# Performance work log

Hardware: AMD Instinct MI355X
Metric: run time of the kernel (lower is better)

## Reference

```python
import jax, jax.numpy as jnp
import numpy as np

B, N = 2, 2048
D_MODEL, HEADS = 512, 8
D_K = D_MODEL // HEADS
D_HIDDEN = 2048
MIN_SPREAD = 2.0
MIN_RBF = 1e-3
MAX_RBF = 1.0
LN_EPS = 1e-5


def setup_inputs() -> dict:
    key = jax.random.key(0)
    ks = jax.random.split(key, 12)
    xs = (6.0 / (D_K + D_MODEL)) ** 0.5
    q = jax.random.normal(ks[0], (B, N, D_MODEL), dtype=jnp.float32)
    k = jax.random.normal(ks[1], (B, N, D_MODEL), dtype=jnp.float32)
    v = jax.random.normal(ks[2], (B, N, D_MODEL), dtype=jnp.float32)
    coords = jax.random.normal(ks[3], (B, N, 3), dtype=jnp.float32) * 10.0
    mask = jnp.ones((B, N), dtype=bool)
    q_proj = jax.random.uniform(ks[4], (HEADS, D_MODEL, D_K), minval=-xs, maxval=xs)
    k_proj = jax.random.uniform(ks[5], (HEADS, D_MODEL, D_K), minval=-xs, maxval=xs)
    v_proj = jax.random.uniform(ks[6], (HEADS, D_MODEL, D_K), minval=-xs, maxval=xs)
    q_bias = jnp.zeros((HEADS, D_K))
    k_bias = jnp.zeros((HEADS, D_K))
    v_bias = jnp.zeros((HEADS, D_K))
    ow = (1.0 / D_MODEL) ** 0.5
    out_w = jax.random.uniform(ks[7], (D_MODEL, D_MODEL), minval=-ow, maxval=ow)
    spread_w = jnp.zeros((HEADS,))
    beta_w = jnp.zeros((HEADS,))
    ln1_g = jnp.ones((D_MODEL,)); ln1_b = jnp.zeros((D_MODEL,))
    ln2_g = jnp.ones((D_MODEL,)); ln2_b = jnp.zeros((D_MODEL,))
    w1 = jax.random.normal(ks[8], (D_MODEL, D_HIDDEN)) * 0.02
    b1 = jnp.zeros((D_HIDDEN,))
    w2 = jax.random.normal(ks[9], (D_HIDDEN, D_MODEL)) * 0.02
    b2 = jnp.zeros((D_MODEL,))
    return dict(q=q, k=k, v=v, coords=coords, mask=mask,
                q_proj=q_proj, k_proj=k_proj, v_proj=v_proj,
                q_bias=q_bias, k_bias=k_bias, v_bias=v_bias,
                out_w=out_w, spread_w=spread_w, beta_w=beta_w,
                ln1_g=ln1_g, ln1_b=ln1_b, ln2_g=ln2_g, ln2_b=ln2_b,
                w1=w1, b1=b1, w2=w2, b2=b2)


def _layernorm(x, g, b):
    mu = jnp.mean(x, axis=-1, keepdims=True)
    var = jnp.mean((x - mu) ** 2, axis=-1, keepdims=True)
    return (x - mu) * jax.lax.rsqrt(var + LN_EPS) * g + b


def _geo_attention(q, k, v, coords, mask,
                   q_proj, k_proj, v_proj, q_bias, k_bias, v_bias,
                   out_w, spread_w, beta_w):
    # per-head projections: [B,H,N,dk]
    Q = jnp.einsum('bnd,hdk->bhnk', q, q_proj) + q_bias[None, :, None, :]
    K = jnp.einsum('bnd,hdk->bhnk', k, k_proj) + k_bias[None, :, None, :]
    V = jnp.einsum('bnd,hdk->bhnk', v, v_proj) + v_bias[None, :, None, :]

    spreads = MIN_SPREAD + jnp.exp(spread_w)   # [H]
    betas = jnp.exp(beta_w)                    # [H]

    # pairwise squared distances [B,N,N]
    d2 = jnp.sum((coords[:, :, None, :] - coords[:, None, :, :]) ** 2, axis=-1)
    # per-head Gaussian RBF [B,H,N,N]
    rbf = jnp.exp(-d2[:, None, :, :] / (2.0 * spreads[None, :, None, None] ** 2))

    scores = jnp.einsum('bhnk,bhmk->bhnm', Q, K) / jnp.sqrt(jnp.float32(D_K))
    scores = betas[None, :, None, None] * rbf * scores

    # sparsity: keys with rbf outside [min_rbf, max_rbf] or padded are masked out
    valid = (rbf >= MIN_RBF) & (rbf <= MAX_RBF) & mask[:, None, None, :]
    scores = jnp.where(valid, scores, -jnp.inf)
    attn = jax.nn.softmax(scores, axis=-1)     # diagonal always valid (rbf=1)

    out = jnp.einsum('bhnm,bhmk->bhnk', attn, V)         # [B,H,N,dk]
    # torch: out.permute(0,2,3,1).reshape(B,N,d_model) -> (b,n,dk,h) layout
    out = jnp.transpose(out, (0, 2, 3, 1)).reshape(out.shape[0], out.shape[2], D_MODEL)
    return out @ out_w.T


def reference(q, k, v, coords, mask,
              q_proj, k_proj, v_proj, q_bias, k_bias, v_bias,
              out_w, spread_w, beta_w,
              ln1_g, ln1_b, ln2_g, ln2_b, w1, b1, w2, b2):
    attn_out = _geo_attention(q, k, v, coords, mask,
                              q_proj, k_proj, v_proj, q_bias, k_bias, v_bias,
                              out_w, spread_w, beta_w)
    x = _layernorm(q + attn_out, ln1_g, ln1_b)
    ffn = jax.nn.relu(x @ w1 + b1) @ w2 + b2
    x = _layernorm(x + ffn, ln2_g, ln2_b)
    return x
```

## Files before the change

kernel.cpp:

```cpp
#include <hip/hip_runtime.h>
#include <math.h>

typedef __attribute__((ext_vector_type(8))) short bf16x8;
typedef __attribute__((ext_vector_type(4))) float f32x4;

#define MFMA16(a,b,c) __builtin_amdgcn_mfma_f32_16x16x32_bf16((a),(b),(c),0,0,0)

__device__ __forceinline__ unsigned short f2bf(float f) {
    union { float f; unsigned u; } x; x.f = f;
    unsigned r = x.u + 0x7FFFu + ((x.u >> 16) & 1u);
    return (unsigned short)(r >> 16);
}

__device__ __forceinline__ unsigned cvt_pk_bf16(float lo, float hi) {
    unsigned r;
    asm("v_cvt_pk_bf16_f32 %0, %1, %2" : "=v"(r) : "v"(lo), "v"(hi));
    return r;
}

__global__ __launch_bounds__(256) void cvt_qkv(
    const float* __restrict__ q, const float* __restrict__ k,
    const float* __restrict__ v,
    unsigned short* __restrict__ qb, unsigned short* __restrict__ kb,
    unsigned short* __restrict__ vb, int n)
{
    for (int i = blockIdx.x * 256 + threadIdx.x; i < n; i += gridDim.x * 256) {
        qb[i] = f2bf(q[i]); kb[i] = f2bf(k[i]); vb[i] = f2bf(v[i]);
    }
}

__global__ __launch_bounds__(256) void cvt_weights(
    const float* __restrict__ qp, const float* __restrict__ kp,
    const float* __restrict__ vp, const float* __restrict__ ow,
    const float* __restrict__ w1, const float* __restrict__ w2,
    const float* __restrict__ qbias, const float* __restrict__ kbias,
    const float* __restrict__ vbias,
    unsigned short* __restrict__ qpT, unsigned short* __restrict__ kpT,
    unsigned short* __restrict__ vpT, unsigned short* __restrict__ owT,
    unsigned short* __restrict__ w1T, unsigned short* __restrict__ w2T,
    float* __restrict__ biasC)
{
    const int NP = 262144;
    const int total = 4 * NP + 1048576 + 1048576 + 1536;
    for (int i = blockIdx.x * 256 + threadIdx.x; i < total; i += gridDim.x * 256) {
        if (i < 3 * NP) {
            int which = i / NP, r = i - which * NP;
            int n = r >> 9, d = r & 511;
            int h = n >> 6, kk = n & 63;
            const float* src = (which == 0) ? qp : (which == 1) ? kp : vp;
            unsigned short* dst = (which == 0) ? qpT : (which == 1) ? kpT : vpT;
            dst[r] = f2bf(src[(h << 15) + (d << 6) + kk]);
        } else if (i < 4 * NP) {
            int r = i - 3 * NP;
            int oi = r >> 9, f = r & 511;
            int h = f >> 6, kk = f & 63;
            owT[r] = f2bf(ow[(oi << 9) + (kk << 3) + h]);
        } else if (i < 4 * NP + 1048576) {
            int r = i - 4 * NP;
            int n = r >> 9, d = r & 511;
            w1T[r] = f2bf(w1[(d << 11) + n]);
        } else if (i < 4 * NP + 2097152) {
            int r = i - 4 * NP - 1048576;
            int n = r >> 11, d = r & 2047;
            w2T[r] = f2bf(w2[(d << 9) + n]);
        } else {
            int j = i - 4 * NP - 2097152;
            biasC[j] = (j < 512) ? qbias[j] : (j < 1024) ? kbias[j - 512] : vbias[j - 1024];
        }
    }
}

template<int BNT, int RELU, int SF32, int SB16, int SVTR, int SQKV>
__global__ __launch_bounds__(256) void gemm_bt(
    const unsigned short* __restrict__ Aq,
    const unsigned short* __restrict__ Ak,
    const unsigned short* __restrict__ Av,
    const unsigned short* __restrict__ Bt,
    const float* __restrict__ bias,
    float* __restrict__ Cf, unsigned short* __restrict__ Cb,
    unsigned short* __restrict__ Cb2, unsigned short* __restrict__ Cb3,
    int M, int N, int K)
{
    constexpr int BC = BNT / 32;
    __shared__ unsigned short As[128][72];
    __shared__ unsigned short Bs[BNT][72];
    const int tid = threadIdx.x;
    const int m0 = blockIdx.y << 7, n0 = blockIdx.x * BNT;
    const int wv = tid >> 6, lane = tid & 63;
    const int lrow = lane & 15, kg = lane >> 4;
    const int wr = (wv >> 1) << 6, wc = (wv & 1) * (BNT / 2);

    const unsigned short* A = Aq;
    if (SQKV) A = (n0 < 512) ? Aq : (n0 < 1024) ? Ak : Av;

    f32x4 acc[4][BC];
    const f32x4 z4 = {0.f, 0.f, 0.f, 0.f};
#pragma unroll
    for (int i = 0; i < 4; ++i)
#pragma unroll
        for (int j = 0; j < BC; ++j) acc[i][j] = z4;

    const int nkt = K >> 6;
    for (int kt = 0; kt < nkt; ++kt) {
        __syncthreads();
        const int k0 = kt << 6;
#pragma unroll
        for (int i = 0; i < 4; ++i) {
            int slot = tid + (i << 8);
            int r = slot >> 3, c = (slot & 7) << 3;
            *(int4*)(&As[r][c]) = *(const int4*)(&A[(long)(m0 + r) * K + k0 + c]);
        }
#pragma unroll
        for (int i = 0; i < BC; ++i) {
            int slot = tid + (i << 8);
            int r = slot >> 3, c = (slot & 7) << 3;
            *(int4*)(&Bs[r][c]) = *(const int4*)(&Bt[(long)(n0 + r) * K + k0 + c]);
        }
        __syncthreads();
#pragma unroll
        for (int ks = 0; ks < 2; ++ks) {
            const int koff = (ks << 5) + (kg << 3);
            bf16x8 af[4], bfr[BC];
#pragma unroll
            for (int mi = 0; mi < 4; ++mi)
                af[mi] = *(const bf16x8*)(&As[wr + (mi << 4) + lrow][koff]);
#pragma unroll
            for (int ni = 0; ni < BC; ++ni)
                bfr[ni] = *(const bf16x8*)(&Bs[wc + (ni << 4) + lrow][koff]);
#pragma unroll
            for (int mi = 0; mi < 4; ++mi)
#pragma unroll
                for (int ni = 0; ni < BC; ++ni)
                    acc[mi][ni] = MFMA16(af[mi], bfr[ni], acc[mi][ni]);
        }
    }

#pragma unroll
    for (int mi = 0; mi < 4; ++mi) {
#pragma unroll
        for (int ni = 0; ni < BC; ++ni) {
            const int col = n0 + wc + (ni << 4) + lrow;
            const float bv = bias ? bias[col] : 0.0f;
#pragma unroll
            for (int j = 0; j < 4; ++j) {
                const int row = m0 + wr + (mi << 4) + (kg << 2) + j;
                float val = acc[mi][ni][j] + bv;
                if (RELU) val = fmaxf(val, 0.0f);
                if (SF32) Cf[(long)row * N + col] = val;
                if (SB16) Cb[(long)row * N + col] = f2bf(val);
                if (SVTR)
                    Cb[((long)(row >> 11) << 20) + ((long)col << 11) + (row & 2047)] = f2bf(val);
                if (SQKV) {
                    if (n0 < 512)
                        Cb[(long)row * 512 + col] = f2bf(val);
                    else if (n0 < 1024)
                        Cb2[(long)row * 512 + (col - 512)] = f2bf(val);
                    else {
                        const int c2 = col - 1024;
                        Cb3[((long)(row >> 11) << 20) + ((long)c2 << 11) + (row & 2047)] = f2bf(val);
                    }
                }
            }
        }
    }
}

__global__ __launch_bounds__(256) void geo_attn(
    const unsigned short* __restrict__ Qh,
    const unsigned short* __restrict__ Kh,
    const unsigned short* __restrict__ VhT,
    const float* __restrict__ coords,
    const float* __restrict__ spread_w, const float* __restrict__ beta_w,
    unsigned short* __restrict__ Ob)
{
    __shared__ unsigned short Qs[64][72];
    __shared__ unsigned short Ks[64][72];
    __shared__ unsigned short Vs[64][72];
    __shared__ unsigned short Ps[4][16][72];
    __shared__ float4 ck4[64];

    const int tid = threadIdx.x;
    const int bid = blockIdx.x;
    const int swz = ((bid & 7) << 6) + (bid >> 3);
    const int bh = swz >> 5, qt = swz & 31;
    const int b = bh >> 3, h = bh & 7;
    const int wv = tid >> 6, lane = tid & 63;
    const int lq = lane & 15, kg = lane >> 4;
    const float NEG_INF = -__builtin_inff();

    const float spread = 2.0f + __expf(spread_w[h]);
    const float inv2s2 = 1.0f / (2.0f * spread * spread);
    const float coef = __expf(beta_w[h]) * 0.125f;

    {
        const long qbase = ((long)(b * 2048 + qt * 64)) * 512 + h * 64;
#pragma unroll
        for (int i = 0; i < 2; ++i) {
            int slot = tid + (i << 8);
            int r = slot >> 3, c = (slot & 7) << 3;
            *(int4*)(&Qs[r][c]) = *(const int4*)(&Qh[qbase + (long)r * 512 + c]);
        }
    }

    float cqx, cqy, cqz;
    {
        long ca = ((long)(b * 2048 + qt * 64 + wv * 16 + lq)) * 3;
        cqx = coords[ca]; cqy = coords[ca + 1]; cqz = coords[ca + 2];
    }

    float mrun = NEG_INF, lrun = 0.0f;
    f32x4 Oa[4];
    const f32x4 z4 = {0.f, 0.f, 0.f, 0.f};
#pragma unroll
    for (int nd = 0; nd < 4; ++nd) Oa[nd] = z4;

    const long kbase0 = ((long)b * 2048) * 512 + h * 64;
    const long vbase = ((long)(b * 8 + h)) * 131072;

    for (int kt = 0; kt < 32; ++kt) {
        __syncthreads();
        const int k0 = kt << 6;
#pragma unroll
        for (int i = 0; i < 2; ++i) {
            int slot = tid + (i << 8);
            int r = slot >> 3, c = (slot & 7) << 3;
            *(int4*)(&Ks[r][c]) = *(const int4*)(&Kh[kbase0 + (long)(k0 + r) * 512 + c]);
            *(int4*)(&Vs[r][c]) = *(const int4*)(&VhT[vbase + (long)r * 2048 + k0 + c]);
        }
        if (tid < 64) {
            long ca = ((long)(b * 2048 + k0 + tid)) * 3;
            ck4[tid] = make_float4(coords[ca], coords[ca + 1], coords[ca + 2], 0.0f);
        }
        __syncthreads();

        f32x4 t4[4];
#pragma unroll
        for (int ra = 0; ra < 4; ++ra) t4[ra] = z4;
#pragma unroll
        for (int ks = 0; ks < 2; ++ks) {
            const int koff = (ks << 5) + (kg << 3);
            bf16x8 bq = *(const bf16x8*)(&Qs[(wv << 4) + lq][koff]);
#pragma unroll
            for (int ra = 0; ra < 4; ++ra) {
                bf16x8 ak = *(const bf16x8*)(&Ks[(ra << 4) + lq][koff]);
                t4[ra] = MFMA16(ak, bq, t4[ra]);
            }
        }

        float tmax = NEG_INF;
#pragma unroll
        for (int ra = 0; ra < 4; ++ra) {
#pragma unroll
            for (int j = 0; j < 4; ++j) {
                float4 ck = ck4[(ra << 4) + (kg << 2) + j];
                float dx = cqx - ck.x, dy = cqy - ck.y, dz = cqz - ck.z;
                float d2 = dx * dx + dy * dy + dz * dz;
                float rbf = __expf(-d2 * inv2s2);
                float val = (rbf >= 1e-3f) ? coef * rbf * t4[ra][j] : NEG_INF;
                t4[ra][j] = val;
                tmax = fmaxf(tmax, val);
            }
        }
        tmax = fmaxf(tmax, __shfl_xor(tmax, 16, 64));
        tmax = fmaxf(tmax, __shfl_xor(tmax, 32, 64));

        const float mn = fmaxf(mrun, tmax);
        const bool dead = (mn == NEG_INF);
        const float mneff = dead ? 0.0f : mn;
        const float fcorr = dead ? 1.0f : __expf(mrun - mn);

        float psum = 0.0f;
#pragma unroll
        for (int ra = 0; ra < 4; ++ra) {
#pragma unroll
            for (int j = 0; j < 4; ++j) {
                float p = __expf(t4[ra][j] - mneff);
                t4[ra][j] = p;
                psum += p;
            }
        }
        psum += __shfl_xor(psum, 16, 64);
        psum += __shfl_xor(psum, 32, 64);
        mrun = mn;
        lrun = lrun * fcorr + psum;

#pragma unroll
        for (int ra = 0; ra < 4; ++ra) {
            uint2 pk;
            pk.x = cvt_pk_bf16(t4[ra][0], t4[ra][1]);
            pk.y = cvt_pk_bf16(t4[ra][2], t4[ra][3]);
            *(uint2*)(&Ps[wv][lq][(ra << 4) + (kg << 2)]) = pk;
        }

        float fb[4];
#pragma unroll
        for (int j = 0; j < 4; ++j)
            fb[j] = __shfl(fcorr, (lane & 48) | ((kg << 2) + j), 64);
#pragma unroll
        for (int nd = 0; nd < 4; ++nd)
#pragma unroll
            for (int j = 0; j < 4; ++j)
                Oa[nd][j] *= fb[j];

#pragma unroll
        for (int ks = 0; ks < 2; ++ks) {
            const int koff = (ks << 5) + (kg << 3);
            bf16x8 ap = *(const bf16x8*)(&Ps[wv][lq][koff]);
#pragma unroll
            for (int nd = 0; nd < 4; ++nd) {
                bf16x8 bv = *(const bf16x8*)(&Vs[(nd << 4) + lq][koff]);
                Oa[nd] = MFMA16(ap, bv, Oa[nd]);
            }
        }
    }

    const float inv = 1.0f / lrun;
    float il[4];
#pragma unroll
    for (int j = 0; j < 4; ++j)
        il[j] = __shfl(inv, (lane & 48) | ((kg << 2) + j), 64);
    const long obase = ((long)(b * 2048 + qt * 64 + (wv << 4))) * 512 + h * 64;
#pragma unroll
    for (int nd = 0; nd < 4; ++nd)
#pragma unroll
        for (int j = 0; j < 4; ++j)
            Ob[obase + (long)((kg << 2) + j) * 512 + (nd << 4) + lq] =
                f2bf(Oa[nd][j] * il[j]);
}

template<int SB16>
__global__ __launch_bounds__(256) void ln_res(
    const float* __restrict__ X, const float* __restrict__ R,
    const float* __restrict__ g, const float* __restrict__ bb,
    float* __restrict__ Yf, unsigned short* __restrict__ Yb)
{
    const int wv = threadIdx.x >> 6, lane = threadIdx.x & 63;
    const long row = (long)blockIdx.x * 4 + wv;
    const float* xp = X + row * 512;
    const float* rp = R + row * 512;
    const int c0 = lane * 8;
    float4 a0 = *(const float4*)(xp + c0);
    float4 a1 = *(const float4*)(xp + c0 + 4);
    float4 r0 = *(const float4*)(rp + c0);
    float4 r1 = *(const float4*)(rp + c0 + 4);
    float v[8] = {a0.x + r0.x, a0.y + r0.y, a0.z + r0.z, a0.w + r0.w,
                  a1.x + r1.x, a1.y + r1.y, a1.z + r1.z, a1.w + r1.w};
    float s = 0.f, ss = 0.f;
#pragma unroll
    for (int i = 0; i < 8; ++i) { s += v[i]; ss += v[i] * v[i]; }
#pragma unroll
    for (int off = 1; off < 64; off <<= 1) {
        s += __shfl_xor(s, off, 64);
        ss += __shfl_xor(ss, off, 64);
    }
    const float mu = s * (1.0f / 512.0f);
    const float var = ss * (1.0f / 512.0f) - mu * mu;
    const float rstd = rsqrtf(var + 1e-5f);
#pragma unroll
    for (int i = 0; i < 8; ++i) {
        const int c = c0 + i;
        const float y = (v[i] - mu) * rstd * g[c] + bb[c];
        Yf[row * 512 + c] = y;
        if (SB16) Yb[row * 512 + c] = f2bf(y);
    }
}

extern "C" void kernel_launch(void* const* d_in, const int* in_sizes, int n_in,
                              void* d_out, int out_size, void* d_ws, size_t ws_size,
                              hipStream_t stream)
{
    const float* q      = (const float*)d_in[0];
    const float* k      = (const float*)d_in[1];
    const float* v      = (const float*)d_in[2];
    const float* coords = (const float*)d_in[3];
    const float* q_proj = (const float*)d_in[5];
    const float* k_proj = (const float*)d_in[6];
    const float* v_proj = (const float*)d_in[7];
    const float* q_bias = (const float*)d_in[8];
    const float* k_bias = (const float*)d_in[9];
    const float* v_bias = (const float*)d_in[10];
    const float* out_w  = (const float*)d_in[11];
    const float* spread_w = (const float*)d_in[12];
    const float* beta_w = (const float*)d_in[13];
    const float* ln1_g  = (const float*)d_in[14];
    const float* ln1_b  = (const float*)d_in[15];
    const float* ln2_g  = (const float*)d_in[16];
    const float* ln2_b  = (const float*)d_in[17];
    const float* w1     = (const float*)d_in[18];
    const float* b1     = (const float*)d_in[19];
    const float* w2     = (const float*)d_in[20];
    const float* b2     = (const float*)d_in[21];
    float* out = (float*)d_out;

    char* ws = (char*)d_ws;
    size_t off = 0;
    auto alloc = [&](size_t bytes) -> void* {
        void* p = ws + off;
        off += (bytes + 255) & ~(size_t)255;
        return p;
    };
    unsigned short* qb   = (unsigned short*)alloc(4096UL * 512 * 2);
    unsigned short* kb   = (unsigned short*)alloc(4096UL * 512 * 2);
    unsigned short* vb   = (unsigned short*)alloc(4096UL * 512 * 2);
    unsigned short* qpT  = (unsigned short*)alloc(512UL * 512 * 2);
    unsigned short* kpT  = (unsigned short*)alloc(512UL * 512 * 2);
    unsigned short* vpT  = (unsigned short*)alloc(512UL * 512 * 2);
    unsigned short* owT  = (unsigned short*)alloc(512UL * 512 * 2);
    unsigned short* w1T  = (unsigned short*)alloc(2048UL * 512 * 2);
    unsigned short* w2T  = (unsigned short*)alloc(512UL * 2048 * 2);
    float* biasC = (float*)alloc(1536UL * 4);
    unsigned short* Qp   = (unsigned short*)alloc(4096UL * 512 * 2);
    unsigned short* Kp   = (unsigned short*)alloc(4096UL * 512 * 2);
    unsigned short* VpT  = (unsigned short*)alloc(4096UL * 512 * 2);
    unsigned short* attnb= (unsigned short*)alloc(4096UL * 512 * 2);
    float* proj = (float*)alloc(4096UL * 512 * 4);
    float* x1   = (float*)alloc(4096UL * 512 * 4);
    unsigned short* x1b = (unsigned short*)alloc(4096UL * 512 * 2);
    unsigned short* hid = (unsigned short*)alloc(4096UL * 2048 * 2);
    float* ffn  = (float*)alloc(4096UL * 512 * 4);
    (void)ws_size; (void)in_sizes; (void)n_in; (void)out_size;

    cvt_qkv<<<2048, 256, 0, stream>>>(q, k, v, qb, kb, vb, 2097152);
    cvt_weights<<<2048, 256, 0, stream>>>(q_proj, k_proj, v_proj, out_w, w1, w2,
                                          q_bias, k_bias, v_bias,
                                          qpT, kpT, vpT, owT, w1T, w2T, biasC);

    gemm_bt<128, 0, 0, 0, 0, 1><<<dim3(12, 32), 256, 0, stream>>>(
        qb, kb, vb, qpT, biasC, nullptr, Qp, Kp, VpT, 4096, 1536, 512);

    geo_attn<<<512, 256, 0, stream>>>(Qp, Kp, VpT, coords, spread_w, beta_w, attnb);

    gemm_bt<64, 0, 1, 0, 0, 0><<<dim3(8, 32), 256, 0, stream>>>(
        attnb, nullptr, nullptr, owT, nullptr, proj, nullptr, nullptr, nullptr, 4096, 512, 512);
    ln_res<1><<<1024, 256, 0, stream>>>(proj, q, ln1_g, ln1_b, x1, x1b);

    gemm_bt<128, 1, 0, 1, 0, 0><<<dim3(16, 32), 256, 0, stream>>>(
        x1b, nullptr, nullptr, w1T, b1, nullptr, hid, nullptr, nullptr, 4096, 2048, 512);
    gemm_bt<64, 0, 1, 0, 0, 0><<<dim3(8, 32), 256, 0, stream>>>(
        hid, nullptr, nullptr, w2T, b2, ffn, nullptr, nullptr, nullptr, 4096, 512, 2048);
    ln_res<0><<<1024, 256, 0, stream>>>(ffn, x1, ln2_g, ln2_b, out, nullptr);
}
```

Baseline: 202.5 us.

## Use direct global-to-LDS loads in GEMM and lazy rescaling with exp2 in attention

```diff
diff --git a/kernel.cpp b/kernel.cpp
--- a/kernel.cpp
+++ b/kernel.cpp
@@ -5,6 +5,7 @@
 typedef __attribute__((ext_vector_type(4))) float f32x4;
 
 #define MFMA16(a,b,c) __builtin_amdgcn_mfma_f32_16x16x32_bf16((a),(b),(c),0,0,0)
+#define LOG2E 1.44269504f
 
 __device__ __forceinline__ unsigned short f2bf(float f) {
     union { float f; unsigned u; } x; x.f = f;
@@ -16,6 +17,17 @@
     unsigned r;
     asm("v_cvt_pk_bf16_f32 %0, %1, %2" : "=v"(r) : "v"(lo), "v"(hi));
     return r;
+}
+
+__device__ __forceinline__ float exp2_fast(float x) {
+    float r; asm("v_exp_f32 %0, %1" : "=v"(r) : "v"(x)); return r;
+}
+
+__device__ __forceinline__ void gload16(const unsigned short* g, unsigned short* l) {
+    __builtin_amdgcn_global_load_lds(
+        (const __attribute__((address_space(1))) void*)(unsigned long long)g,
+        (__attribute__((address_space(3))) void*)(unsigned int)(unsigned long long)l,
+        16, 0, 0);
 }
 
 __global__ __launch_bounds__(256) void cvt_qkv(
@@ -82,13 +94,14 @@
     int M, int N, int K)
 {
     constexpr int BC = BNT / 32;
-    __shared__ unsigned short As[128][72];
-    __shared__ unsigned short Bs[BNT][72];
+    __shared__ __align__(16) unsigned short As[128][64];
+    __shared__ __align__(16) unsigned short Bs[BNT][64];
     const int tid = threadIdx.x;
     const int m0 = blockIdx.y << 7, n0 = blockIdx.x * BNT;
     const int wv = tid >> 6, lane = tid & 63;
     const int lrow = lane & 15, kg = lane >> 4;
     const int wr = (wv >> 1) << 6, wc = (wv & 1) * (BNT / 2);
+    const int gr = lane >> 3, gc = (lane & 7) << 3;
 
     const unsigned short* A = Aq;
     if (SQKV) A = (n0 < 512) ? Aq : (n0 < 1024) ? Ak : Av;
@@ -106,15 +119,13 @@
         const int k0 = kt << 6;
 #pragma unroll
         for (int i = 0; i < 4; ++i) {
-            int slot = tid + (i << 8);
-            int r = slot >> 3, c = (slot & 7) << 3;
-            *(int4*)(&As[r][c]) = *(const int4*)(&A[(long)(m0 + r) * K + k0 + c]);
-        }
-#pragma unroll
-        for (int i = 0; i < BC; ++i) {
-            int slot = tid + (i << 8);
-            int r = slot >> 3, c = (slot & 7) << 3;
-            *(int4*)(&Bs[r][c]) = *(const int4*)(&Bt[(long)(n0 + r) * K + k0 + c]);
+            const int r = (wv << 5) + (i << 3);
+            gload16(&A[(long)(m0 + r + gr) * K + k0 + gc], &As[r][0]);
+        }
+#pragma unroll
+        for (int i = 0; i < BNT / 32; ++i) {
+            const int r = wv * (BNT / 4) + (i << 3);
+            gload16(&Bt[(long)(n0 + r + gr) * K + k0 + gc], &Bs[r][0]);
         }
         __syncthreads();
 #pragma unroll
@@ -187,10 +198,12 @@
     const int wv = tid >> 6, lane = tid & 63;
     const int lq = lane & 15, kg = lane >> 4;
     const float NEG_INF = -__builtin_inff();
+    const float THRL = 8.0f * LOG2E;
+    const float RCUT = -9.96578428f;
 
     const float spread = 2.0f + __expf(spread_w[h]);
-    const float inv2s2 = 1.0f / (2.0f * spread * spread);
-    const float coef = __expf(beta_w[h]) * 0.125f;
+    const float inv2s2l = LOG2E / (2.0f * spread * spread);
+    const float coefL = __expf(beta_w[h]) * 0.125f * LOG2E;
 
     {
         const long qbase = ((long)(b * 2048 + qt * 64)) * 512 + h * 64;
@@ -255,8 +268,9 @@
                 float4 ck = ck4[(ra << 4) + (kg << 2) + j];
                 float dx = cqx - ck.x, dy = cqy - ck.y, dz = cqz - ck.z;
                 float d2 = dx * dx + dy * dy + dz * dz;
-                float rbf = __expf(-d2 * inv2s2);
-                float val = (rbf >= 1e-3f) ? coef * rbf * t4[ra][j] : NEG_INF;
+                float rexp = -d2 * inv2s2l;
+                float rbf = exp2_fast(rexp);
+                float val = (rexp >= RCUT) ? coefL * rbf * t4[ra][j] : NEG_INF;
                 t4[ra][j] = val;
                 tmax = fmaxf(tmax, val);
             }
@@ -264,25 +278,50 @@
         tmax = fmaxf(tmax, __shfl_xor(tmax, 16, 64));
         tmax = fmaxf(tmax, __shfl_xor(tmax, 32, 64));
 
-        const float mn = fmaxf(mrun, tmax);
-        const bool dead = (mn == NEG_INF);
-        const float mneff = dead ? 0.0f : mn;
-        const float fcorr = dead ? 1.0f : __expf(mrun - mn);
-
+        const bool grow_any = __any(tmax > mrun + THRL);
         float psum = 0.0f;
-#pragma unroll
-        for (int ra = 0; ra < 4; ++ra) {
-#pragma unroll
-            for (int j = 0; j < 4; ++j) {
-                float p = __expf(t4[ra][j] - mneff);
-                t4[ra][j] = p;
-                psum += p;
-            }
-        }
-        psum += __shfl_xor(psum, 16, 64);
-        psum += __shfl_xor(psum, 32, 64);
-        mrun = mn;
-        lrun = lrun * fcorr + psum;
+        if (grow_any) {
+            const float mn = fmaxf(mrun, tmax);
+            const bool dead = (mn == NEG_INF);
+            const float meff = dead ? 0.0f : mn;
+            const float fcorr = dead ? 1.0f : exp2_fast(mrun - mn);
+#pragma unroll
+            for (int ra = 0; ra < 4; ++ra) {
+#pragma unroll
+                for (int j = 0; j < 4; ++j) {
+                    float p = exp2_fast(t4[ra][j] - meff);
+                    t4[ra][j] = p;
+                    psum += p;
+                }
+            }
+            psum += __shfl_xor(psum, 16, 64);
+            psum += __shfl_xor(psum, 32, 64);
+            mrun = mn;
+            lrun = lrun * fcorr + psum;
+            float fb[4];
+#pragma unroll
+            for (int j = 0; j < 4; ++j)
+                fb[j] = __shfl(fcorr, (lane & 48) | ((kg << 2) + j), 64);
+#pragma unroll
+            for (int nd = 0; nd < 4; ++nd)
+#pragma unroll
+                for (int j = 0; j < 4; ++j)
+                    Oa[nd][j] *= fb[j];
+        } else {
+            const float meff = (mrun == NEG_INF) ? 0.0f : mrun;
+#pragma unroll
+            for (int ra = 0; ra < 4; ++ra) {
+#pragma unroll
+                for (int j = 0; j < 4; ++j) {
+                    float p = exp2_fast(t4[ra][j] - meff);
+                    t4[ra][j] = p;
+                    psum += p;
+                }
+            }
+            psum += __shfl_xor(psum, 16, 64);
+            psum += __shfl_xor(psum, 32, 64);
+            lrun += psum;
+        }
 
 #pragma unroll
         for (int ra = 0; ra < 4; ++ra) {
@@ -291,16 +330,6 @@
             pk.y = cvt_pk_bf16(t4[ra][2], t4[ra][3]);
             *(uint2*)(&Ps[wv][lq][(ra << 4) + (kg << 2)]) = pk;
         }
-
-        float fb[4];
-#pragma unroll
-        for (int j = 0; j < 4; ++j)
-            fb[j] = __shfl(fcorr, (lane & 48) | ((kg << 2) + j), 64);
-#pragma unroll
-        for (int nd = 0; nd < 4; ++nd)
-#pragma unroll
-            for (int j = 0; j < 4; ++j)
-                Oa[nd][j] *= fb[j];
 
 #pragma unroll
         for (int ks = 0; ks < 2; ++ks) {
```

New measurement: 211.0 us. 4.2% more time.
